# Optimization experiments

Hardware: AMD Instinct MI355X
Metric: run time of the kernel (lower is better)

The kernel has to match this reference:

```python
import jax, jax.numpy as jnp
import numpy as np


def setup_inputs() -> dict:
    key = jax.random.key(0)
    k1, k2 = jax.random.split(key)
    x = jax.random.normal(k1, (16, 64, 128, 128), dtype=jnp.float32)
    # 1x1 conv weight, no bias: [C_out, C_in]
    conv_w = jax.random.normal(k2, (64, 64), dtype=jnp.float32) * 0.05
    return {"x": x, "conv_w": conv_w}


def reference(x, conv_w):
    B, C, H, W = x.shape
    N = H * W
    xf = x.reshape(B, C, N)  # [B, C, N]
    # Original: f = X^T X  [B,N,N];  y = X @ (f / N).
    # Mathematically identical reassociation (no nonlinearity between matmuls):
    # y = (X X^T) X / N, using a tiny [B,C,C] gram instead of [B,N,N].
    gram = jnp.einsum('bcn,bdn->bcd', xf, xf) / N  # [B, C, C]
    y = jnp.einsum('bcd,bdn->bcn', gram, xf)       # [B, C, N]
    y = y.reshape(B, C, H, W)
    # 1x1 conv, bias=False: channel mixing
    out = jnp.einsum('oc,bchw->bohw', conv_w, y)
    return out
```

## Files before the change

### kernel.cpp

```cpp
#include <hip/hip_runtime.h>

#define B_ 16
#define C_ 64
#define N_ 16384
#define KCH 32
#define CPB 512
#define SROW 72

typedef __attribute__((ext_vector_type(8))) short bf16x8;
typedef __attribute__((ext_vector_type(4))) float f32x4;
typedef __attribute__((ext_vector_type(4))) short s16x4;

__device__ __forceinline__ short f2bf(float f) {
    unsigned int u = __float_as_uint(f);
    unsigned int r = (u + 0x7FFFu + ((u >> 16) & 1u)) >> 16;
    return (short)r;
}

__device__ __forceinline__ bf16x8 cvt8(float4 lo, float4 hi) {
    bf16x8 r;
    r[0] = f2bf(lo.x); r[1] = f2bf(lo.y); r[2] = f2bf(lo.z); r[3] = f2bf(lo.w);
    r[4] = f2bf(hi.x); r[5] = f2bf(hi.y); r[6] = f2bf(hi.z); r[7] = f2bf(hi.w);
    return r;
}

__global__ __launch_bounds__(256)
void gram_kernel(const float* __restrict__ x, float* __restrict__ gpart) {
    __shared__ float red[2][4096];
    const int t = threadIdx.x, l = t & 63, w = t >> 6;
    const int b = blockIdx.y, ch = blockIdx.x;
    const float* xb = x + (size_t)b * (C_ * (size_t)N_);
    const int row = l & 15, kg = l >> 4;
    const int kbase = ch * CPB + w * (CPB / 4);

    f32x4 acc[4][4] = {};
    float4 raw[2][4][2];

    #pragma unroll
    for (int g = 0; g < 4; ++g) {
        const float* p = xb + (size_t)(16 * g + row) * N_ + kbase + kg * 8;
        raw[0][g][0] = *(const float4*)p;
        raw[0][g][1] = *(const float4*)(p + 4);
    }

    #pragma unroll
    for (int ks = 0; ks < 4; ++ks) {
        const int cb = ks & 1, nb = cb ^ 1;
        if (ks < 3) {
            #pragma unroll
            for (int g = 0; g < 4; ++g) {
                const float* p = xb + (size_t)(16 * g + row) * N_ +
                                 kbase + (ks + 1) * 32 + kg * 8;
                raw[nb][g][0] = *(const float4*)p;
                raw[nb][g][1] = *(const float4*)(p + 4);
            }
        }
        bf16x8 fr[4];
        #pragma unroll
        for (int g = 0; g < 4; ++g) fr[g] = cvt8(raw[cb][g][0], raw[cb][g][1]);
        #pragma unroll
        for (int gc = 0; gc < 4; ++gc)
            #pragma unroll
            for (int gd = 0; gd < 4; ++gd)
                acc[gc][gd] = __builtin_amdgcn_mfma_f32_16x16x32_bf16(
                    fr[gc], fr[gd], acc[gc][gd], 0, 0, 0);
    }

    if (w < 2) {
        #pragma unroll
        for (int gc = 0; gc < 4; ++gc)
            #pragma unroll
            for (int gd = 0; gd < 4; ++gd)
                *(f32x4*)&red[w][(gc * 4 + gd) * 256 + l * 4] = acc[gc][gd];
    }
    __syncthreads();
    if (w >= 2) {
        #pragma unroll
        for (int gc = 0; gc < 4; ++gc)
            #pragma unroll
            for (int gd = 0; gd < 4; ++gd) {
                float* p = &red[w - 2][(gc * 4 + gd) * 256 + l * 4];
                f32x4 v = *(f32x4*)p;
                *(f32x4*)p = v + acc[gc][gd];
            }
    }
    __syncthreads();

    f32x4* dst = (f32x4*)(gpart + ((size_t)b * KCH + ch) * 4096);
    const f32x4* r0 = (const f32x4*)red[0];
    const f32x4* r1 = (const f32x4*)red[1];
    #pragma unroll
    for (int j = 0; j < 4; ++j)
        dst[j * 256 + t] = r0[j * 256 + t] + r1[j * 256 + t];
}

__global__ __launch_bounds__(256)
void reduce_kernel(const float* __restrict__ gpart, float* __restrict__ G) {
    const int gid = blockIdx.x * 256 + threadIdx.x;
    const int b = gid >> 12, e = gid & 4095;
    const float* p = gpart + ((size_t)b * KCH) * 4096 + e;
    float s0 = 0.f, s1 = 0.f, s2 = 0.f, s3 = 0.f;
    #pragma unroll
    for (int ch = 0; ch < KCH; ch += 4) {
        s0 += p[(size_t)(ch + 0) * 4096];
        s1 += p[(size_t)(ch + 1) * 4096];
        s2 += p[(size_t)(ch + 2) * 4096];
        s3 += p[(size_t)(ch + 3) * 4096];
    }
    G[gid] = (s0 + s1) + (s2 + s3);
}

__global__ __launch_bounds__(256)
void m_kernel(const float* __restrict__ W, const float* __restrict__ G,
              unsigned short* __restrict__ Mbf) {
    __shared__ float Gs[C_][17];
    __shared__ float Ws[C_][65];
    const int gd = blockIdx.x, b = blockIdx.y, t = threadIdx.x;

    for (int i = t; i < C_ * C_; i += 256) Ws[i >> 6][i & 63] = W[i];

    const int f = t;
    #pragma unroll
    for (int gc = 0; gc < 4; ++gc) {
        float s = G[(size_t)b * 4096 + (gc * 4 + gd) * 256 + f];
        const int c = gc * 16 + (f >> 6) * 4 + (f & 3);
        const int dloc = (f >> 2) & 15;
        Gs[c][dloc] = s;
    }
    __syncthreads();

    const int o = t & 63, g2 = t >> 6;
    const float invN = 1.0f / (float)N_;
    #pragma unroll
    for (int j = 0; j < 4; ++j) {
        const int dloc = g2 * 4 + j;
        float s = 0.f;
        #pragma unroll
        for (int c = 0; c < C_; ++c) s = fmaf(Ws[o][c], Gs[c][dloc], s);
        Mbf[((size_t)b * C_ + o) * C_ + gd * 16 + dloc] = (unsigned short)f2bf(s * invN);
    }
}

__global__ __launch_bounds__(256, 4)
void out_kernel(const float* __restrict__ x, const unsigned short* __restrict__ Mbf,
                float* __restrict__ out) {
    __shared__ unsigned short Xt[256][SROW];
    const int t = threadIdx.x, l = t & 63, w = t >> 6;
    const int b = blockIdx.y, n0 = blockIdx.x * 256;
    const float* xb = x + (size_t)b * (C_ * (size_t)N_);
    const int row = l & 15, kg = l >> 4;

    bf16x8 afrag[2][4];
    #pragma unroll
    for (int ks = 0; ks < 2; ++ks)
        #pragma unroll
        for (int g = 0; g < 4; ++g)
            afrag[ks][g] = *(const bf16x8*)((const short*)Mbf +
                ((size_t)b * C_ + 16 * g + row) * C_ + ks * 32 + kg * 8);

    const int d0 = (t & 15) * 4, nb2 = (t >> 4) * 16;
    #pragma unroll
    for (int p = 0; p < 2; ++p) {
        const int n8 = nb2 + p * 8;
        float a[4][8];
        #pragma unroll
        for (int r = 0; r < 4; ++r) {
            const float* src = xb + (size_t)(d0 + r) * N_ + n0 + n8;
            float4 q0 = *(const float4*)src;
            float4 q1 = *(const float4*)(src + 4);
            a[r][0] = q0.x; a[r][1] = q0.y; a[r][2] = q0.z; a[r][3] = q0.w;
            a[r][4] = q1.x; a[r][5] = q1.y; a[r][6] = q1.z; a[r][7] = q1.w;
        }
        #pragma unroll
        for (int j = 0; j < 8; ++j) {
            s16x4 pk;
            pk[0] = f2bf(a[0][j]); pk[1] = f2bf(a[1][j]);
            pk[2] = f2bf(a[2][j]); pk[3] = f2bf(a[3][j]);
            *(s16x4*)&Xt[n8 + j][d0] = pk;
        }
    }
    __syncthreads();

    float* ob = out + (size_t)b * (C_ * (size_t)N_);
    #pragma unroll
    for (int nt = 0; nt < 4; ++nt) {
        const int ntile = w * 4 + nt;
        bf16x8 bfrag0 = *(const bf16x8*)&Xt[ntile * 16 + row][kg * 8];
        bf16x8 bfrag1 = *(const bf16x8*)&Xt[ntile * 16 + row][32 + kg * 8];
        #pragma unroll
        for (int g = 0; g < 4; ++g) {
            f32x4 acc = {};
            acc = __builtin_amdgcn_mfma_f32_16x16x32_bf16(afrag[0][g], bfrag0, acc, 0, 0, 0);
            acc = __builtin_amdgcn_mfma_f32_16x16x32_bf16(afrag[1][g], bfrag1, acc, 0, 0, 0);
            #pragma unroll
            for (int r = 0; r < 4; ++r)
                ob[(size_t)(16 * g + 4 * kg + r) * N_ + n0 + ntile * 16 + row] = acc[r];
        }
    }
}

extern "C" void kernel_launch(void* const* d_in, const int* in_sizes, int n_in,
                              void* d_out, int out_size, void* d_ws, size_t ws_size,
                              hipStream_t stream) {
    const float* x = (const float*)d_in[0];
    const float* w = (const float*)d_in[1];
    float* out = (float*)d_out;

    float* gpart = (float*)d_ws;
    float* G = gpart + (size_t)B_ * KCH * 4096;
    unsigned short* Mbf = (unsigned short*)(G + (size_t)B_ * 4096);

    gram_kernel<<<dim3(KCH, B_), 256, 0, stream>>>(x, gpart);
    reduce_kernel<<<dim3((B_ * 4096) / 256), 256, 0, stream>>>(gpart, G);
    m_kernel<<<dim3(4, B_), 256, 0, stream>>>(w, G, Mbf);
    out_kernel<<<dim3(N_ / 256, B_), 256, 0, stream>>>(x, Mbf, out);
}
```

Before: 55.28 us.

## Fuse partial-gram reduction into M kernel and batch gram loads upfront

Removes the separate reduce kernel by having the M kernel sum the per-chunk gram partials directly with nontemporal loads, eliminating one launch and the intermediate G buffer. The gram kernel now issues all global loads for its four k-steps before any MFMA instead of double-buffering, raising register use but exposing more memory parallelism. The output kernel writes results with nontemporal stores to avoid cache pollution, and the bf16 conversion uses the HIP library intrinsic. The fused reduction runs on only 64 blocks, which may lengthen that stage.

```diff
diff --git a/kernel.cpp b/kernel.cpp
--- a/kernel.cpp
+++ b/kernel.cpp
@@ -1,4 +1,5 @@
 #include <hip/hip_runtime.h>
+#include <hip/hip_bf16.h>
 
 #define B_ 16
 #define C_ 64
@@ -12,9 +13,7 @@
 typedef __attribute__((ext_vector_type(4))) short s16x4;
 
 __device__ __forceinline__ short f2bf(float f) {
-    unsigned int u = __float_as_uint(f);
-    unsigned int r = (u + 0x7FFFu + ((u >> 16) & 1u)) >> 16;
-    return (short)r;
+    return (short)__bfloat16_as_ushort(__float2bfloat16(f));
 }
 
 __device__ __forceinline__ bf16x8 cvt8(float4 lo, float4 hi) {
@@ -33,31 +32,22 @@
     const int row = l & 15, kg = l >> 4;
     const int kbase = ch * CPB + w * (CPB / 4);
 
+    float4 raw[4][4][2];
+    #pragma unroll
+    for (int ks = 0; ks < 4; ++ks)
+        #pragma unroll
+        for (int g = 0; g < 4; ++g) {
+            const float* p = xb + (size_t)(16 * g + row) * N_ + kbase + ks * 32 + kg * 8;
+            raw[ks][g][0] = *(const float4*)p;
+            raw[ks][g][1] = *(const float4*)(p + 4);
+        }
+
     f32x4 acc[4][4] = {};
-    float4 raw[2][4][2];
-
-    #pragma unroll
-    for (int g = 0; g < 4; ++g) {
-        const float* p = xb + (size_t)(16 * g + row) * N_ + kbase + kg * 8;
-        raw[0][g][0] = *(const float4*)p;
-        raw[0][g][1] = *(const float4*)(p + 4);
-    }
-
     #pragma unroll
     for (int ks = 0; ks < 4; ++ks) {
-        const int cb = ks & 1, nb = cb ^ 1;
-        if (ks < 3) {
-            #pragma unroll
-            for (int g = 0; g < 4; ++g) {
-                const float* p = xb + (size_t)(16 * g + row) * N_ +
-                                 kbase + (ks + 1) * 32 + kg * 8;
-                raw[nb][g][0] = *(const float4*)p;
-                raw[nb][g][1] = *(const float4*)(p + 4);
-            }
-        }
         bf16x8 fr[4];
         #pragma unroll
-        for (int g = 0; g < 4; ++g) fr[g] = cvt8(raw[cb][g][0], raw[cb][g][1]);
+        for (int g = 0; g < 4; ++g) fr[g] = cvt8(raw[ks][g][0], raw[ks][g][1]);
         #pragma unroll
         for (int gc = 0; gc < 4; ++gc)
             #pragma unroll
@@ -95,24 +85,8 @@
 }
 
 __global__ __launch_bounds__(256)
-void reduce_kernel(const float* __restrict__ gpart, float* __restrict__ G) {
-    const int gid = blockIdx.x * 256 + threadIdx.x;
-    const int b = gid >> 12, e = gid & 4095;
-    const float* p = gpart + ((size_t)b * KCH) * 4096 + e;
-    float s0 = 0.f, s1 = 0.f, s2 = 0.f, s3 = 0.f;
-    #pragma unroll
-    for (int ch = 0; ch < KCH; ch += 4) {
-        s0 += p[(size_t)(ch + 0) * 4096];
-        s1 += p[(size_t)(ch + 1) * 4096];
-        s2 += p[(size_t)(ch + 2) * 4096];
-        s3 += p[(size_t)(ch + 3) * 4096];
-    }
-    G[gid] = (s0 + s1) + (s2 + s3);
-}
-
-__global__ __launch_bounds__(256)
-void m_kernel(const float* __restrict__ W, const float* __restrict__ G,
-              unsigned short* __restrict__ Mbf) {
+void rm_kernel(const float* __restrict__ W, const float* __restrict__ gpart,
+               unsigned short* __restrict__ Mbf) {
     __shared__ float Gs[C_][17];
     __shared__ float Ws[C_][65];
     const int gd = blockIdx.x, b = blockIdx.y, t = threadIdx.x;
@@ -122,10 +96,18 @@
     const int f = t;
     #pragma unroll
     for (int gc = 0; gc < 4; ++gc) {
-        float s = G[(size_t)b * 4096 + (gc * 4 + gd) * 256 + f];
+        const float* p = gpart + (size_t)b * KCH * 4096 + (gc * 4 + gd) * 256 + f;
+        float s0 = 0.f, s1 = 0.f, s2 = 0.f, s3 = 0.f;
+        #pragma unroll 2
+        for (int ch = 0; ch < KCH; ch += 4) {
+            s0 += __builtin_nontemporal_load(&p[(size_t)(ch + 0) * 4096]);
+            s1 += __builtin_nontemporal_load(&p[(size_t)(ch + 1) * 4096]);
+            s2 += __builtin_nontemporal_load(&p[(size_t)(ch + 2) * 4096]);
+            s3 += __builtin_nontemporal_load(&p[(size_t)(ch + 3) * 4096]);
+        }
         const int c = gc * 16 + (f >> 6) * 4 + (f & 3);
         const int dloc = (f >> 2) & 15;
-        Gs[c][dloc] = s;
+        Gs[c][dloc] = (s0 + s1) + (s2 + s3);
     }
     __syncthreads();
 
@@ -194,7 +176,8 @@
             acc = __builtin_amdgcn_mfma_f32_16x16x32_bf16(afrag[1][g], bfrag1, acc, 0, 0, 0);
             #pragma unroll
             for (int r = 0; r < 4; ++r)
-                ob[(size_t)(16 * g + 4 * kg + r) * N_ + n0 + ntile * 16 + row] = acc[r];
+                __builtin_nontemporal_store(acc[r],
+                    &ob[(size_t)(16 * g + 4 * kg + r) * N_ + n0 + ntile * 16 + row]);
         }
     }
 }
@@ -207,11 +190,9 @@
     float* out = (float*)d_out;
 
     float* gpart = (float*)d_ws;
-    float* G = gpart + (size_t)B_ * KCH * 4096;
-    unsigned short* Mbf = (unsigned short*)(G + (size_t)B_ * 4096);
+    unsigned short* Mbf = (unsigned short*)(gpart + (size_t)B_ * KCH * 4096);
 
     gram_kernel<<<dim3(KCH, B_), 256, 0, stream>>>(x, gpart);
-    reduce_kernel<<<dim3((B_ * 4096) / 256), 256, 0, stream>>>(gpart, G);
-    m_kernel<<<dim3(4, B_), 256, 0, stream>>>(w, G, Mbf);
+    rm_kernel<<<dim3(4, B_), 256, 0, stream>>>(w, gpart, Mbf);
     out_kernel<<<dim3(N_ / 256, B_), 256, 0, stream>>>(x, Mbf, out);
 }
```

Measured after the change: 60.25 us. 1.09x slower.
